# Kernel optimization log

Hardware: AMD Instinct MI355X
Metric: run time of the kernel (lower is better)

Reference implementation:

```python
import jax, jax.numpy as jnp
import numpy as np

N = 512  # n_vertices (batch size whose pairwise distances are given)


def _persistence_pairs(D):
    """0-dim persistence pairs = MST edges of the complete graph (Kruskal).
    Faithful to PersistentHomologyCalculation: stable sort over upper-tri
    (incl. diagonal) edge weights, union-find with the same merge direction.
    Returns (pu, pv) each of shape [n-1] with pu < pv, in acceptance order."""
    n = D.shape[0]
    rows_np, cols_np = np.triu_indices(n)  # matches torch.triu_indices(n, n)
    rows = jnp.asarray(rows_np, jnp.int32)
    cols = jnp.asarray(cols_np, jnp.int32)
    w = D[rows, cols]
    order = jnp.argsort(w, stable=True)
    eu = rows[order]
    ev = cols[order]

    def find(parent, x):
        # path-halving find (equivalent roots to recursive path compression)
        def cond(state):
            p, y = state
            return p[y] != y
        def body(state):
            p, y = state
            gp = p[p[y]]
            p = p.at[y].set(gp)
            return (p, gp)
        return jax.lax.while_loop(cond, body, (parent, x))

    def step(carry, edge):
        parent, pu, pv, count = carry
        u, v = edge
        parent, ru = find(parent, u)
        parent, rv = find(parent, v)
        valid = ru != rv
        # younger (larger root) merges into older, matching the torch code
        tgt = jnp.where(ru > rv, rv, ru)
        val = jnp.where(ru > rv, ru, rv)
        parent = parent.at[tgt].set(jnp.where(valid, val, parent[tgt]))
        idx = jnp.minimum(count, n - 2)  # only n-1 edges are ever accepted
        lo = jnp.minimum(u, v)
        hi = jnp.maximum(u, v)
        pu = pu.at[idx].set(jnp.where(valid, lo, pu[idx]))
        pv = pv.at[idx].set(jnp.where(valid, hi, pv[idx]))
        count = count + valid.astype(count.dtype)
        return (parent, pu, pv, count), None

    init = (jnp.arange(n, dtype=jnp.int32),
            jnp.zeros(n - 1, jnp.int32),
            jnp.zeros(n - 1, jnp.int32),
            jnp.int32(0))
    (_, pu, pv, _), _ = jax.lax.scan(step, init, (eu, ev))
    return pu, pv


def _pairwise_dist(X):
    sq = jnp.sum((X[:, None, :] - X[None, :, :]) ** 2, axis=-1)
    return jnp.sqrt(jnp.maximum(sq, 0.0))


def setup_inputs() -> dict:
    key = jax.random.key(0)
    k1, k2 = jax.random.split(key)
    X1 = jax.random.normal(k1, (N, 16), dtype=jnp.float32)
    X2 = jax.random.normal(k2, (N, 16), dtype=jnp.float32)
    return {"distances1": _pairwise_dist(X1), "distances2": _pairwise_dist(X2)}


def reference(distances1, distances2):
    # match_edges == 'symmetric'
    p1u, p1v = _persistence_pairs(distances1)
    p2u, p2v = _persistence_pairs(distances2)
    sig1 = distances1[p1u, p1v]
    sig1_2 = distances2[p1u, p1v]
    sig2 = distances2[p2u, p2v]
    sig2_1 = distances1[p2u, p2v]
    distance1_2 = jnp.sum((sig1 - sig1_2) ** 2)
    distance2_1 = jnp.sum((sig2 - sig2_1) ** 2)
    return distance1_2 + distance2_1
```

## Files before the change

kernel.cpp:

```cpp
#include <hip/hip_runtime.h>

namespace {

constexpr int NV = 512;
typedef unsigned long long ull;
constexpr ull INF64 = ~0ULL;

__global__ __launch_bounds__(1024) void boruvka_loss(
    const float* __restrict__ d1, const float* __restrict__ d2,
    float* __restrict__ partial)
{
    const int blk = blockIdx.x;
    const float* __restrict__ Dm = blk ? d2 : d1;
    const float* __restrict__ Do = blk ? d1 : d2;
    const int tid = threadIdx.x;

    __shared__ unsigned comp[NV];
    __shared__ ull      best[NV];
    __shared__ unsigned parent[NV];
    __shared__ int      accTot;
    __shared__ float    red[1024];

    if (tid < NV) comp[tid] = tid;
    if (tid == 0) accTot = 0;

    float myContrib = 0.f;

    const int v  = tid >> 1;
    const int c0 = (tid & 1) << 8;
    const float* __restrict__ rowp = Dm + ((size_t)v << 9) + c0;

    for (int round = 0; round < 10; ++round) {
        if (tid < NV) best[tid] = INF64;
        __syncthreads();

        {
            const unsigned cv = comp[v];
            unsigned wmin = 0xFFFFFFFFu;
            unsigned umin = 0;
            bool any = false;
#pragma unroll 4
            for (int s = 0; s < 256; s += 4) {
                float4 w4 = *reinterpret_cast<const float4*>(rowp + s);
                uint4  q4 = *reinterpret_cast<const uint4*>(&comp[c0 + s]);
                unsigned wb;
                wb = __float_as_uint(w4.x);
                if ((q4.x != cv) && (!any || wb < wmin)) { wmin = wb; umin = c0 + s + 0; any = true; }
                wb = __float_as_uint(w4.y);
                if ((q4.y != cv) && (wb < wmin || !any)) { wmin = wb; umin = c0 + s + 1; any = true; }
                wb = __float_as_uint(w4.z);
                if ((q4.z != cv) && (wb < wmin || !any)) { wmin = wb; umin = c0 + s + 2; any = true; }
                wb = __float_as_uint(w4.w);
                if ((q4.w != cv) && (wb < wmin || !any)) { wmin = wb; umin = c0 + s + 3; any = true; }
            }
            if (any) {
                unsigned uv = (unsigned)v;
                unsigned lo = (umin < uv) ? ((umin << 9) | uv) : ((uv << 9) | umin);
                atomicMin(&best[cv], ((ull)wmin << 32) | lo);
            }
        }
        __syncthreads();

        if (tid < NV) {
            ull e = best[tid];
            unsigned p = tid;
            if (e != INF64) {
                unsigned lo = (unsigned)e & 0x3FFFFu;
                unsigned i = lo >> 9, j = lo & 511u;
                unsigned ci = comp[i], cj = comp[j];
                p = (ci == (unsigned)tid) ? cj : ci;
            }
            parent[tid] = p;
        }
        __syncthreads();

        if (tid < NV) {
            unsigned p = parent[tid];
            if (p != (unsigned)tid && parent[p] == (unsigned)tid && (unsigned)tid < p)
                parent[tid] = tid;
        }
        __syncthreads();

        if (tid < NV) {
            ull e = best[tid];
            if (e != INF64) {
                unsigned lo = (unsigned)e & 0x3FFFFu;
                unsigned i = lo >> 9, j = lo & 511u;
                unsigned ci = comp[i], cj = comp[j];
                unsigned p = (ci == (unsigned)tid) ? cj : ci;
                bool dup = (best[p] == e) && (p < (unsigned)tid);
                if (!dup) {
                    float a  = __uint_as_float((unsigned)(e >> 32));
                    float bo = Do[(size_t)i * NV + j];
                    float d = a - bo;
                    myContrib += d * d;
                    atomicAdd(&accTot, 1);
                }
            }
        }

        for (int jt = 0; jt < 9; ++jt) {
            __syncthreads();
            if (tid < NV) parent[tid] = parent[parent[tid]];
        }
        __syncthreads();

        if (tid < NV) comp[tid] = parent[comp[tid]];
        __syncthreads();

        if (accTot == NV - 1) break;
    }

    red[tid] = myContrib;
    for (int off = 512; off >= 1; off >>= 1) {
        __syncthreads();
        if (tid < off) red[tid] += red[tid + off];
    }
    if (tid == 0) partial[blk] = red[0];
}

__global__ void final_add(const float* __restrict__ partial, float* __restrict__ out) {
    out[0] = partial[0] + partial[1];
}

}

extern "C" void kernel_launch(void* const* d_in, const int* in_sizes, int n_in,
                              void* d_out, int out_size, void* d_ws, size_t ws_size,
                              hipStream_t stream) {
    const float* d1 = (const float*)d_in[0];
    const float* d2 = (const float*)d_in[1];
    float* out = (float*)d_out;
    float* ws = (float*)d_ws;

    boruvka_loss<<<2, 1024, 0, stream>>>(d1, d2, ws);
    final_add<<<1, 1, 0, stream>>>(ws, out);
}
```

Measured before the change: 97.29 us.

## Move Boruvka merge phase into a single wavefront to drop block barriers

The component-merge, cycle-breaking, edge-accounting and pointer-jumping phases now run inside one 64-lane wavefront, with block-scoped fences instead of many block-wide __syncthreads per round. The per-row min search becomes a branchless 4-way min that records the winning chunk and resolves the exact column afterwards, and the final reduction uses wave shuffles rather than a shared-memory tree. Accepted edges are counted with a ballot and popcount instead of a shared atomic. The aim is to cut barrier latency in this small two-block, latency-bound kernel, at the cost of serialising the merge work onto fewer threads.

```diff
diff --git a/kernel.cpp b/kernel.cpp
--- a/kernel.cpp
+++ b/kernel.cpp
@@ -5,6 +5,7 @@
 constexpr int NV = 512;
 typedef unsigned long long ull;
 constexpr ull INF64 = ~0ULL;
+constexpr unsigned WMAX = 0xFFFFFFFFu;
 
 __global__ __launch_bounds__(1024) void boruvka_loss(
     const float* __restrict__ d1, const float* __restrict__ d2,
@@ -14,109 +15,134 @@
     const float* __restrict__ Dm = blk ? d2 : d1;
     const float* __restrict__ Do = blk ? d1 : d2;
     const int tid = threadIdx.x;
+    const int lane = tid & 63;
 
-    __shared__ unsigned comp[NV];
-    __shared__ ull      best[NV];
+    __shared__ __align__(16) unsigned comp[NV];
+    __shared__ ull best[NV];
     __shared__ unsigned parent[NV];
-    __shared__ int      accTot;
-    __shared__ float    red[1024];
+    __shared__ int doneFlag;
 
-    if (tid < NV) comp[tid] = tid;
-    if (tid == 0) accTot = 0;
-
-    float myContrib = 0.f;
+    if (tid < NV) { comp[tid] = tid; best[tid] = INF64; }
+    if (tid == 0) doneFlag = 0;
 
     const int v  = tid >> 1;
     const int c0 = (tid & 1) << 8;
-    const float* __restrict__ rowp = Dm + ((size_t)v << 9) + c0;
+    const float4* __restrict__ rowp4 =
+        reinterpret_cast<const float4*>(Dm + ((size_t)v << 9) + c0);
+    const uint4* comp4 = reinterpret_cast<const uint4*>(&comp[c0]);
 
-    for (int round = 0; round < 10; ++round) {
-        if (tid < NV) best[tid] = INF64;
-        __syncthreads();
+    float contrib = 0.f;
+    int accTotal = 0;
 
+    __syncthreads();
+
+    for (int round = 0; round < 9; ++round) {
         {
             const unsigned cv = comp[v];
-            unsigned wmin = 0xFFFFFFFFu;
-            unsigned umin = 0;
-            bool any = false;
-#pragma unroll 4
-            for (int s = 0; s < 256; s += 4) {
-                float4 w4 = *reinterpret_cast<const float4*>(rowp + s);
-                uint4  q4 = *reinterpret_cast<const uint4*>(&comp[c0 + s]);
-                unsigned wb;
-                wb = __float_as_uint(w4.x);
-                if ((q4.x != cv) && (!any || wb < wmin)) { wmin = wb; umin = c0 + s + 0; any = true; }
-                wb = __float_as_uint(w4.y);
-                if ((q4.y != cv) && (wb < wmin || !any)) { wmin = wb; umin = c0 + s + 1; any = true; }
-                wb = __float_as_uint(w4.z);
-                if ((q4.z != cv) && (wb < wmin || !any)) { wmin = wb; umin = c0 + s + 2; any = true; }
-                wb = __float_as_uint(w4.w);
-                if ((q4.w != cv) && (wb < wmin || !any)) { wmin = wb; umin = c0 + s + 3; any = true; }
+            unsigned wmin = WMAX;
+            int smin = 0;
+#pragma unroll 8
+            for (int s = 0; s < 64; ++s) {
+                float4 w4 = rowp4[s];
+                uint4  q4 = comp4[s];
+                unsigned m0 = (q4.x != cv) ? __float_as_uint(w4.x) : WMAX;
+                unsigned m1 = (q4.y != cv) ? __float_as_uint(w4.y) : WMAX;
+                unsigned m2 = (q4.z != cv) ? __float_as_uint(w4.z) : WMAX;
+                unsigned m3 = (q4.w != cv) ? __float_as_uint(w4.w) : WMAX;
+                unsigned t = min(min(m0, m1), min(m2, m3));
+                if (t < wmin) { wmin = t; smin = s; }
             }
-            if (any) {
+            if (wmin != WMAX) {
+                float4 w4 = rowp4[smin];
+                uint4  q4 = comp4[smin];
+                unsigned m0 = (q4.x != cv) ? __float_as_uint(w4.x) : WMAX;
+                unsigned m1 = (q4.y != cv) ? __float_as_uint(w4.y) : WMAX;
+                unsigned m2 = (q4.z != cv) ? __float_as_uint(w4.z) : WMAX;
+                int k = (m0 == wmin) ? 0 : (m1 == wmin) ? 1 : (m2 == wmin) ? 2 : 3;
+                unsigned umin = (unsigned)(c0 + smin * 4 + k);
                 unsigned uv = (unsigned)v;
                 unsigned lo = (umin < uv) ? ((umin << 9) | uv) : ((uv << 9) | umin);
-                atomicMin(&best[cv], ((ull)wmin << 32) | lo);
+                atomicMin(&best[cv], ((ull)wmin << 32) | (ull)lo);
             }
         }
         __syncthreads();
 
-        if (tid < NV) {
-            ull e = best[tid];
-            unsigned p = tid;
-            if (e != INF64) {
-                unsigned lo = (unsigned)e & 0x3FFFFu;
-                unsigned i = lo >> 9, j = lo & 511u;
-                unsigned ci = comp[i], cj = comp[j];
-                p = (ci == (unsigned)tid) ? cj : ci;
+        if (tid < 64) {
+#pragma unroll
+            for (int k = 0; k < 8; ++k) {
+                int t = lane + 64 * k;
+                ull e = best[t];
+                unsigned p = (unsigned)t;
+                if (e != INF64) {
+                    unsigned j = (unsigned)e & 511u;
+                    unsigned i = ((unsigned)e >> 9) & 511u;
+                    unsigned ci = comp[i], cj = comp[j];
+                    p = (ci == (unsigned)t) ? cj : ci;
+                }
+                parent[t] = p;
             }
-            parent[tid] = p;
+            __threadfence_block();
+
+#pragma unroll
+            for (int k = 0; k < 8; ++k) {
+                int t = lane + 64 * k;
+                unsigned p = parent[t];
+                if (p != (unsigned)t && parent[p] == (unsigned)t && (unsigned)t < p)
+                    parent[t] = (unsigned)t;
+            }
+            __threadfence_block();
+
+            int accRound = 0;
+#pragma unroll
+            for (int k = 0; k < 8; ++k) {
+                int t = lane + 64 * k;
+                ull e = best[t];
+                bool take = false;
+                unsigned i = 0, j = 0;
+                if (e != INF64) {
+                    j = (unsigned)e & 511u;
+                    i = ((unsigned)e >> 9) & 511u;
+                    unsigned ci = comp[i], cj = comp[j];
+                    unsigned p = (ci == (unsigned)t) ? cj : ci;
+                    take = !((best[p] == e) && (p < (unsigned)t));
+                }
+                if (take) {
+                    float a = __uint_as_float((unsigned)(e >> 32));
+                    float b = Do[((size_t)i << 9) + j];
+                    float d = a - b;
+                    contrib += d * d;
+                }
+                accRound += __popcll(__ballot(take));
+            }
+            accTotal += accRound;
+            __threadfence_block();
+
+            for (int jt = 0; jt < 9; ++jt) {
+#pragma unroll
+                for (int k = 0; k < 8; ++k) {
+                    int t = lane + 64 * k;
+                    parent[t] = parent[parent[t]];
+                }
+                __threadfence_block();
+            }
+
+#pragma unroll
+            for (int k = 0; k < 8; ++k) {
+                int t = lane + 64 * k;
+                comp[t] = parent[comp[t]];
+                best[t] = INF64;
+            }
+            if (lane == 0) doneFlag = (accTotal == NV - 1) ? 1 : 0;
         }
         __syncthreads();
-
-        if (tid < NV) {
-            unsigned p = parent[tid];
-            if (p != (unsigned)tid && parent[p] == (unsigned)tid && (unsigned)tid < p)
-                parent[tid] = tid;
-        }
-        __syncthreads();
-
-        if (tid < NV) {
-            ull e = best[tid];
-            if (e != INF64) {
-                unsigned lo = (unsigned)e & 0x3FFFFu;
-                unsigned i = lo >> 9, j = lo & 511u;
-                unsigned ci = comp[i], cj = comp[j];
-                unsigned p = (ci == (unsigned)tid) ? cj : ci;
-                bool dup = (best[p] == e) && (p < (unsigned)tid);
-                if (!dup) {
-                    float a  = __uint_as_float((unsigned)(e >> 32));
-                    float bo = Do[(size_t)i * NV + j];
-                    float d = a - bo;
-                    myContrib += d * d;
-                    atomicAdd(&accTot, 1);
-                }
-            }
-        }
-
-        for (int jt = 0; jt < 9; ++jt) {
-            __syncthreads();
-            if (tid < NV) parent[tid] = parent[parent[tid]];
-        }
-        __syncthreads();
-
-        if (tid < NV) comp[tid] = parent[comp[tid]];
-        __syncthreads();
-
-        if (accTot == NV - 1) break;
+        if (doneFlag) break;
     }
 
-    red[tid] = myContrib;
-    for (int off = 512; off >= 1; off >>= 1) {
-        __syncthreads();
-        if (tid < off) red[tid] += red[tid + off];
+    if (tid < 64) {
+#pragma unroll
+        for (int off = 32; off >= 1; off >>= 1) contrib += __shfl_xor(contrib, off);
+        if (lane == 0) partial[blk] = contrib;
     }
-    if (tid == 0) partial[blk] = red[0];
 }
 
 __global__ void final_add(const float* __restrict__ partial, float* __restrict__ out) {
```

Measured after the change: 181.2 us. +86.2%, slower.

## Replace pointer-jumping barrier loop with root chase and wave-level counting

Applied to the files above, without the earlier changes.

Each thread now chases its component's root in the parent forest directly, replacing the nine barrier-separated pointer-jumping steps per Boruvka round. The shared atomic edge counter becomes a per-wave ballot popcount summed by one thread. The final block reduction moves from a 1024-entry shared tree to wave shuffles. The best-edge reset is folded into the end-of-round barrier, and the loaded best entry is reused across phases. This cuts the number of block-wide barriers per round. The trade-off is possibly divergent while-loops when the parent chains are deep.

```diff
diff --git a/kernel.cpp b/kernel.cpp
--- a/kernel.cpp
+++ b/kernel.cpp
@@ -5,6 +5,7 @@
 constexpr int NV = 512;
 typedef unsigned long long ull;
 constexpr ull INF64 = ~0ULL;
+constexpr unsigned WMAX = 0xFFFFFFFFu;
 
 __global__ __launch_bounds__(1024) void boruvka_loss(
     const float* __restrict__ d1, const float* __restrict__ d2,
@@ -14,109 +15,118 @@
     const float* __restrict__ Dm = blk ? d2 : d1;
     const float* __restrict__ Do = blk ? d1 : d2;
     const int tid = threadIdx.x;
+    const int lane = tid & 63;
+    const int wid = tid >> 6;
 
-    __shared__ unsigned comp[NV];
-    __shared__ ull      best[NV];
+    __shared__ __align__(16) unsigned comp[NV];
+    __shared__ ull best[NV];
     __shared__ unsigned parent[NV];
-    __shared__ int      accTot;
-    __shared__ float    red[1024];
+    __shared__ int waveAcc[16];
+    __shared__ float red[16];
+    __shared__ int accTot;
 
-    if (tid < NV) comp[tid] = tid;
+    if (tid < NV) { comp[tid] = tid; best[tid] = INF64; }
     if (tid == 0) accTot = 0;
-
-    float myContrib = 0.f;
 
     const int v  = tid >> 1;
     const int c0 = (tid & 1) << 8;
-    const float* __restrict__ rowp = Dm + ((size_t)v << 9) + c0;
+    const float4* __restrict__ rowp4 =
+        reinterpret_cast<const float4*>(Dm + ((size_t)v << 9) + c0);
+    const uint4* comp4 = reinterpret_cast<const uint4*>(&comp[c0]);
+
+    float contrib = 0.f;
+
+    __syncthreads();
 
     for (int round = 0; round < 10; ++round) {
-        if (tid < NV) best[tid] = INF64;
-        __syncthreads();
-
         {
             const unsigned cv = comp[v];
-            unsigned wmin = 0xFFFFFFFFu;
-            unsigned umin = 0;
+            unsigned wmin = WMAX, umin = 0;
             bool any = false;
 #pragma unroll 4
-            for (int s = 0; s < 256; s += 4) {
-                float4 w4 = *reinterpret_cast<const float4*>(rowp + s);
-                uint4  q4 = *reinterpret_cast<const uint4*>(&comp[c0 + s]);
+            for (int s = 0; s < 64; ++s) {
+                float4 w4 = rowp4[s];
+                uint4  q4 = comp4[s];
                 unsigned wb;
                 wb = __float_as_uint(w4.x);
-                if ((q4.x != cv) && (!any || wb < wmin)) { wmin = wb; umin = c0 + s + 0; any = true; }
+                if ((q4.x != cv) && (!any || wb < wmin)) { wmin = wb; umin = c0 + s*4 + 0; any = true; }
                 wb = __float_as_uint(w4.y);
-                if ((q4.y != cv) && (wb < wmin || !any)) { wmin = wb; umin = c0 + s + 1; any = true; }
+                if ((q4.y != cv) && (wb < wmin || !any)) { wmin = wb; umin = c0 + s*4 + 1; any = true; }
                 wb = __float_as_uint(w4.z);
-                if ((q4.z != cv) && (wb < wmin || !any)) { wmin = wb; umin = c0 + s + 2; any = true; }
+                if ((q4.z != cv) && (wb < wmin || !any)) { wmin = wb; umin = c0 + s*4 + 2; any = true; }
                 wb = __float_as_uint(w4.w);
-                if ((q4.w != cv) && (wb < wmin || !any)) { wmin = wb; umin = c0 + s + 3; any = true; }
+                if ((q4.w != cv) && (wb < wmin || !any)) { wmin = wb; umin = c0 + s*4 + 3; any = true; }
             }
             if (any) {
                 unsigned uv = (unsigned)v;
                 unsigned lo = (umin < uv) ? ((umin << 9) | uv) : ((uv << 9) | umin);
-                atomicMin(&best[cv], ((ull)wmin << 32) | lo);
+                atomicMin(&best[cv], ((ull)wmin << 32) | (ull)lo);
             }
         }
         __syncthreads();
 
+        ull he = INF64; unsigned hp = 0, hlo = 0;
         if (tid < NV) {
-            ull e = best[tid];
-            unsigned p = tid;
-            if (e != INF64) {
-                unsigned lo = (unsigned)e & 0x3FFFFu;
-                unsigned i = lo >> 9, j = lo & 511u;
-                unsigned ci = comp[i], cj = comp[j];
-                p = (ci == (unsigned)tid) ? cj : ci;
+            unsigned t = (unsigned)tid;
+            he = best[t];
+            hp = t;
+            if (he != INF64) {
+                hlo = (unsigned)he & 0x3FFFFu;
+                unsigned ci = comp[hlo >> 9], cj = comp[hlo & 511u];
+                hp = (ci == t) ? cj : ci;
             }
-            parent[tid] = p;
+            parent[t] = hp;
         }
         __syncthreads();
 
         if (tid < NV) {
-            unsigned p = parent[tid];
-            if (p != (unsigned)tid && parent[p] == (unsigned)tid && (unsigned)tid < p)
-                parent[tid] = tid;
+            unsigned t = (unsigned)tid, p = parent[t];
+            if (p != t && parent[p] == t && t < p) parent[t] = t;
         }
         __syncthreads();
 
-        if (tid < NV) {
-            ull e = best[tid];
-            if (e != INF64) {
-                unsigned lo = (unsigned)e & 0x3FFFFu;
-                unsigned i = lo >> 9, j = lo & 511u;
-                unsigned ci = comp[i], cj = comp[j];
-                unsigned p = (ci == (unsigned)tid) ? cj : ci;
-                bool dup = (best[p] == e) && (p < (unsigned)tid);
-                if (!dup) {
-                    float a  = __uint_as_float((unsigned)(e >> 32));
-                    float bo = Do[(size_t)i * NV + j];
-                    float d = a - bo;
-                    myContrib += d * d;
-                    atomicAdd(&accTot, 1);
-                }
+        bool take = false;
+        if (tid < NV && he != INF64) {
+            take = !((best[hp] == he) && (hp < (unsigned)tid));
+            if (take) {
+                float a = __uint_as_float((unsigned)(he >> 32));
+                float b = Do[hlo];
+                float d = a - b;
+                contrib += d * d;
             }
         }
-
-        for (int jt = 0; jt < 9; ++jt) {
-            __syncthreads();
-            if (tid < NV) parent[tid] = parent[parent[tid]];
+        {
+            ull bal = __ballot(take);
+            if (lane == 0) waveAcc[wid] = __popcll(bal);
+        }
+        if (tid < NV) {
+            unsigned r = comp[tid];
+            while (parent[r] != r) r = parent[r];
+            comp[tid] = r;
         }
         __syncthreads();
 
-        if (tid < NV) comp[tid] = parent[comp[tid]];
+        if (tid < NV) best[tid] = INF64;
+        if (tid == 0) {
+            int s = 0;
+#pragma unroll
+            for (int w = 0; w < 16; ++w) s += waveAcc[w];
+            accTot += s;
+        }
         __syncthreads();
-
         if (accTot == NV - 1) break;
     }
 
-    red[tid] = myContrib;
-    for (int off = 512; off >= 1; off >>= 1) {
-        __syncthreads();
-        if (tid < off) red[tid] += red[tid + off];
+#pragma unroll
+    for (int off = 32; off >= 1; off >>= 1) contrib += __shfl_xor(contrib, off);
+    if (lane == 0) red[wid] = contrib;
+    __syncthreads();
+    if (tid == 0) {
+        float s = 0.f;
+#pragma unroll
+        for (int w = 0; w < 16; ++w) s += red[w];
+        partial[blk] = s;
     }
-    if (tid == 0) partial[blk] = red[0];
 }
 
 __global__ void final_add(const float* __restrict__ partial, float* __restrict__ out) {
```

Measured after the change: 167.5 us. 1.72x slower.
